# Performance work log

Hardware: AMD Instinct MI355X
Metric: run time of the kernel (lower is better)

## Reference

```python
import jax, jax.numpy as jnp
import numpy as np
from jax import lax

B, QL, VL, D, H, K = 8, 512, 2048, 1024, 8, 10
DH = D // H  # per-head dim = 128


def setup_inputs() -> dict:
    key = jax.random.key(0)
    ks = jax.random.split(key, 12)
    s = 0.02
    return {
        "Q": jax.random.normal(ks[0], (B, QL, D), jnp.float32),
        "V": jax.random.normal(ks[1], (B, VL, D), jnp.float32),
        "last_align": jax.random.uniform(ks[2], (B, QL), jnp.float32),
        "conv_w": jax.random.normal(ks[3], (K, 1, 3), jnp.float32) * s,
        "conv_b": jnp.zeros((K,), jnp.float32),
        "Wq": jax.random.normal(ks[4], (D, D), jnp.float32) * s,
        "bq": jnp.zeros((D,), jnp.float32),
        "Wv": jax.random.normal(ks[5], (D, D), jnp.float32) * s,
        "bv": jnp.zeros((D,), jnp.float32),
        "Wu": jax.random.normal(ks[6], (D, K), jnp.float32) * s,
        "bu": jnp.zeros((D,), jnp.float32),
        "bias": jax.random.uniform(ks[7], (D,), jnp.float32, -0.1, 0.1),
        "fc_w": jax.random.normal(ks[8], (D, 2 * D), jnp.float32) * s,
        "fc_b": jnp.zeros((D,), jnp.float32),
    }


def reference(Q, V, last_align, conv_w, conv_b, Wq, bq, Wv, bv, Wu, bu, bias, fc_w, fc_b):
    b, qlen, d_model = Q.shape
    vlen = V.shape[1]
    # location feature: conv1d over last_align -> (B, K, qlen) -> (B, qlen, K)
    u = lax.conv_general_dilated(last_align[:, None, :], conv_w, (1,), [(1, 1)],
                                 dimension_numbers=("NCH", "OIH", "NCH"))
    U = jnp.transpose(u + conv_b[None, :, None], (0, 2, 1))  # (B, qlen, K)
    # fused projections + bias adds
    q_s = Q @ Wq.T + bq + U @ Wu.T + bu + bias  # (B, qlen, D)
    v_s = V @ Wv.T + bv                          # (B, vlen, D)
    q_s = q_s.reshape(b, qlen, H, DH)
    v_s = v_s.reshape(b, vlen, H, DH)
    score = jnp.einsum("bqhd,bvhd->bhqv", q_s, v_s) / np.sqrt(DH).astype(jnp.float32)
    # sigmoid smoothing normalization (not softmax)
    score = jax.nn.sigmoid(score)
    align = score / jnp.sum(score, axis=-1, keepdims=True)  # (B, H, qlen, vlen)
    context = jnp.einsum("bhqv,bvhd->bqhd", align, v_s).reshape(b, qlen, d_model)
    combined = jnp.concatenate([context, Q], axis=-1)  # (B, qlen, 2D)
    output = jnp.tanh(combined @ fc_w.T + fc_b)        # (B, qlen, D)
    # torch returns align flattened head-major: (H*B, qlen, vlen)
    align_t = jnp.transpose(align, (1, 0, 2, 3)).reshape(H * b, qlen, vlen)
    return output, align_t
```

## Files before the change

kernel.cpp:

```cpp
#include <hip/hip_runtime.h>

typedef __attribute__((ext_vector_type(8))) short short8;
typedef __attribute__((ext_vector_type(4))) short short4v;
typedef __attribute__((ext_vector_type(4))) float f32x4;

static __device__ __forceinline__ short f2bf(float x) {
    unsigned u = __builtin_bit_cast(unsigned, x);
    unsigned r = (u + 0x7fffu + ((u >> 16) & 1u)) >> 16;
    return (short)r;
}

static __device__ __forceinline__ void gld16(const short* g, short* l) {
    __builtin_amdgcn_global_load_lds((const __attribute__((address_space(1))) void*)g,
                                     (__attribute__((address_space(3))) void*)l, 16, 0, 0);
}

#define QL 512
#define VL 2048
#define DM 1024
#define NH 8
#define DH 128
#define NB 8
#define KQ 1088

__global__ void cbias_k(const float* __restrict__ bq, const float* __restrict__ bu,
                        const float* __restrict__ bias, float* __restrict__ cbias) {
    int i = blockIdx.x * 256 + threadIdx.x;
    if (i < DM) cbias[i] = bq[i] + bu[i] + bias[i];
}

__global__ void conv_prep_k(const float* __restrict__ la, const float* __restrict__ cw,
                            const float* __restrict__ cb, short* __restrict__ Aq) {
    int m = blockIdx.x * 256 + threadIdx.x;
    if (m >= NB * QL) return;
    int b = m >> 9, t = m & 511;
    const float* l = la + b * QL;
    float lm = (t > 0)      ? l[t - 1] : 0.f;
    float l0 = l[t];
    float lp = (t < QL - 1) ? l[t + 1] : 0.f;
    short* row = Aq + (size_t)m * KQ + 1024;
#pragma unroll
    for (int k = 0; k < 10; ++k)
        row[k] = f2bf(cb[k] + lm * cw[k * 3 + 0] + l0 * cw[k * 3 + 1] + lp * cw[k * 3 + 2]);
    for (int k = 10; k < 64; ++k) row[k] = 0;
}

__global__ void castq_k(const float* __restrict__ Q, short* __restrict__ Aq,
                        short* __restrict__ comb) {
    int id = blockIdx.x * 256 + threadIdx.x;
    int m = id >> 7, kc = (id & 127) * 8;
    const float* p = Q + (size_t)m * DM + kc;
    float4 f0 = *(const float4*)p;
    float4 f1 = *(const float4*)(p + 4);
    short8 v;
    v[0]=f2bf(f0.x); v[1]=f2bf(f0.y); v[2]=f2bf(f0.z); v[3]=f2bf(f0.w);
    v[4]=f2bf(f1.x); v[5]=f2bf(f1.y); v[6]=f2bf(f1.z); v[7]=f2bf(f1.w);
    *(short8*)(Aq + (size_t)m * KQ + kc) = v;
    *(short8*)(comb + (size_t)m * (2 * DM) + DM + kc) = v;
}

__global__ void castv_k(const float* __restrict__ V, short* __restrict__ Vb) {
    int id = blockIdx.x * 256 + threadIdx.x;
    const float* p = V + (size_t)id * 8;
    float4 f0 = *(const float4*)p;
    float4 f1 = *(const float4*)(p + 4);
    short8 v;
    v[0]=f2bf(f0.x); v[1]=f2bf(f0.y); v[2]=f2bf(f0.z); v[3]=f2bf(f0.w);
    v[4]=f2bf(f1.x); v[5]=f2bf(f1.y); v[6]=f2bf(f1.z); v[7]=f2bf(f1.w);
    *(short8*)(Vb + (size_t)id * 8) = v;
}

__global__ void buildw_k(const float* __restrict__ Wq, const float* __restrict__ Wu,
                         const float* __restrict__ Wv, const float* __restrict__ fcw,
                         short* __restrict__ Bq, short* __restrict__ Bv, short* __restrict__ Bfc) {
    int id = blockIdx.x * 256 + threadIdx.x;
    const int nq = DM * KQ;
    const int nv = DM * DM;
    const int nf = DM * 2 * DM;
    if (id < nq) {
        int n = id / KQ, k = id % KQ;
        float v = (k < 1024) ? Wq[(size_t)n * 1024 + k]
                             : ((k < 1034) ? Wu[n * 10 + (k - 1024)] : 0.f);
        Bq[id] = f2bf(v);
    } else if (id < nq + nv) {
        int j = id - nq;
        Bv[j] = f2bf(Wv[j]);
    } else if (id < nq + nv + nf) {
        int j = id - nq - nv;
        Bfc[j] = f2bf(fcw[j]);
    }
}

template <int MODE>
__global__ __launch_bounds__(256) void gemm2_k(
    const short* __restrict__ A, const short* __restrict__ B,
    const float* __restrict__ bias, void* __restrict__ out0,
    short* __restrict__ outT, int M, int N, int K, int out_ld) {
    __shared__ short As[128 * 64];
    __shared__ short Bs[128 * 64];
    const int tid = threadIdx.x;
    const int lane = tid & 63, wave = tid >> 6;
    const int g = lane >> 4, c = lane & 15;
    const int nbm = M >> 7;
    const int x = blockIdx.x & 7, j = blockIdx.x >> 3;
    const int bm = x * (nbm >> 3) + (j >> 3);
    const int bn = j & 7;
    const int wr = wave >> 1, wc = wave & 1;

    const int srow = lane >> 3, scol = (lane & 7) * 8;
    const short* ag = A + (size_t)(bm * 128 + wave * 32 + srow) * K + scol;
    const short* bg = B + (size_t)(bn * 128 + wave * 32 + srow) * K + scol;

    f32x4 acc[4][4] = {};
    for (int k0 = 0; k0 < K; k0 += 64) {
#pragma unroll
        for (int ch = 0; ch < 4; ++ch) {
            gld16(ag + (size_t)(ch * 8) * K + k0, As + (wave * 32 + ch * 8) * 64);
            gld16(bg + (size_t)(ch * 8) * K + k0, Bs + (wave * 32 + ch * 8) * 64);
        }
        __syncthreads();
#pragma unroll
        for (int ks = 0; ks < 2; ++ks) {
            short8 af[4], bfr[4];
#pragma unroll
            for (int mi = 0; mi < 4; ++mi) af[mi] = *(const short8*)(As + (wr * 64 + mi * 16 + c) * 64 + ks * 32 + g * 8);
#pragma unroll
            for (int ni = 0; ni < 4; ++ni) bfr[ni] = *(const short8*)(Bs + (wc * 64 + ni * 16 + c) * 64 + ks * 32 + g * 8);
#pragma unroll
            for (int mi = 0; mi < 4; ++mi)
#pragma unroll
                for (int ni = 0; ni < 4; ++ni)
                    acc[mi][ni] = __builtin_amdgcn_mfma_f32_16x16x32_bf16(af[mi], bfr[ni], acc[mi][ni], 0, 0, 0);
        }
        __syncthreads();
    }

    const int m0 = bm * 128 + wr * 64, n0 = bn * 128 + wc * 64;
#pragma unroll
    for (int ni = 0; ni < 4; ++ni) {
        int n = n0 + ni * 16 + c;
        float bn_ = bias[n];
#pragma unroll
        for (int mi = 0; mi < 4; ++mi) {
            int mb = m0 + mi * 16 + 4 * g;
            f32x4 v = acc[mi][ni];
            if constexpr (MODE == 2) {
                float* o = (float*)out0;
#pragma unroll
                for (int r = 0; r < 4; ++r)
                    o[(size_t)(mb + r) * out_ld + n] = tanhf(v[r] + bn_);
            } else {
                short* o = (short*)out0;
                short4v pk;
#pragma unroll
                for (int r = 0; r < 4; ++r) {
                    pk[r] = f2bf(v[r] + bn_);
                    o[(size_t)(mb + r) * out_ld + n] = pk[r];
                }
                if constexpr (MODE == 0) {
                    int h = n >> 7, hd = n & 127;
                    int bb = mb >> 11, vv = mb & 2047;
                    *(short4v*)(outT + ((size_t)((bb * NH + h) * DH + hd)) * VL + vv) = pk;
                }
            }
        }
    }
}

__global__ __launch_bounds__(256) void rowsum_k(
    const short* __restrict__ qs, const short* __restrict__ vs,
    float* __restrict__ rsum_part) {
    __shared__ short As[128 * 64];
    __shared__ short Bs[128 * 64];
    const int blk = blockIdx.x;
    const int xr = blk & 7, t = blk >> 3;
    const int bn = t & 15;
    const int bm = (t >> 4) & 3;
    const int bh = ((t >> 6) << 3) | xr;
    const int h = bh & 7, b = bh >> 3;

    const int tid = threadIdx.x;
    const int lane = tid & 63, wave = tid >> 6;
    const int g = lane >> 4, c = lane & 15;
    const int wr = wave >> 1, wc = wave & 1;
    const float sc = 0.08838834764831845f;

    const int srow = lane >> 3, scol = (lane & 7) * 8;
    const short* ag = qs + (size_t)(b * QL + bm * 128 + wave * 32 + srow) * DM + h * DH + scol;
    const short* bg = vs + (size_t)(b * VL + bn * 128 + wave * 32 + srow) * DM + h * DH + scol;

    f32x4 acc[4][4] = {};
    for (int k0 = 0; k0 < DH; k0 += 64) {
#pragma unroll
        for (int ch = 0; ch < 4; ++ch) {
            gld16(ag + (size_t)(ch * 8) * DM + k0, As + (wave * 32 + ch * 8) * 64);
            gld16(bg + (size_t)(ch * 8) * DM + k0, Bs + (wave * 32 + ch * 8) * 64);
        }
        __syncthreads();
#pragma unroll
        for (int ks = 0; ks < 2; ++ks) {
            short8 af[4], bfr[4];
#pragma unroll
            for (int mi = 0; mi < 4; ++mi) af[mi] = *(const short8*)(As + (wr * 64 + mi * 16 + c) * 64 + ks * 32 + g * 8);
#pragma unroll
            for (int ni = 0; ni < 4; ++ni) bfr[ni] = *(const short8*)(Bs + (wc * 64 + ni * 16 + c) * 64 + ks * 32 + g * 8);
#pragma unroll
            for (int mi = 0; mi < 4; ++mi)
#pragma unroll
                for (int ni = 0; ni < 4; ++ni)
                    acc[mi][ni] = __builtin_amdgcn_mfma_f32_16x16x32_bf16(af[mi], bfr[ni], acc[mi][ni], 0, 0, 0);
        }
        __syncthreads();
    }

    float psum[4][4];
#pragma unroll
    for (int mi = 0; mi < 4; ++mi)
#pragma unroll
        for (int r = 0; r < 4; ++r) psum[mi][r] = 0.f;

    const int m0 = bm * 128 + wr * 64;
#pragma unroll
    for (int ni = 0; ni < 4; ++ni) {
#pragma unroll
        for (int mi = 0; mi < 4; ++mi) {
            f32x4 v = acc[mi][ni];
#pragma unroll
            for (int r = 0; r < 4; ++r)
                psum[mi][r] += __builtin_amdgcn_rcpf(1.f + __expf(-v[r] * sc));
        }
    }
#pragma unroll
    for (int off = 1; off < 16; off <<= 1)
#pragma unroll
        for (int mi = 0; mi < 4; ++mi)
#pragma unroll
            for (int r = 0; r < 4; ++r) psum[mi][r] += __shfl_xor(psum[mi][r], off);
    if (c == 0) {
#pragma unroll
        for (int mi = 0; mi < 4; ++mi)
#pragma unroll
            for (int r = 0; r < 4; ++r) {
                int q = m0 + mi * 16 + 4 * g + r;
                rsum_part[(size_t)(bh * QL + q) * 32 + bn * 2 + wc] = psum[mi][r];
            }
    }
}

__global__ __launch_bounds__(256) void fat_k(
    const short* __restrict__ qs, const short* __restrict__ vs,
    const short* __restrict__ vsT, const float* __restrict__ rsum_part,
    float* __restrict__ align_out, short* __restrict__ comb) {
    __shared__ short Vs[64][136];
    __shared__ short Vt[128][72];
    __shared__ short Pl[4][16][72];
    __shared__ float rsl[64];

    const int blk = blockIdx.x;
    const int xr = blk & 7, t = blk >> 3;
    const int qt = t & 7;
    const int bh = ((t >> 3) << 3) | xr;
    const int h = bh & 7, b = bh >> 3;
    const int q0 = qt * 64;

    const int tid = threadIdx.x, wave = tid >> 6, lane = tid & 63;
    const int g = lane >> 4, c = lane & 15;
    const float sc = 0.08838834764831845f;

    if (tid < 64) {
        const float* p = rsum_part + (size_t)(bh * QL + q0 + tid) * 32;
        float s = 0.f;
#pragma unroll
        for (int jj = 0; jj < 32; ++jj) s += p[jj];
        rsl[tid] = __builtin_amdgcn_rcpf(s);
    }
    __syncthreads();

    float invr[4];
#pragma unroll
    for (int r = 0; r < 4; ++r) invr[r] = rsl[wave * 16 + 4 * g + r];

    short8 qa[4];
    const short* qb = qs + ((size_t)(b * QL + q0 + wave * 16 + c)) * DM + h * DH + g * 8;
#pragma unroll
    for (int ks = 0; ks < 4; ++ks) qa[ks] = *(const short8*)(qb + ks * 32);

    const int vsrow = tid >> 2, vscq = (tid & 3) * 32;
    const short* vsg = vs + ((size_t)(b * VL + vsrow)) * DM + h * DH + vscq;
    const int vtrow = tid >> 1, vtcq = (tid & 1) * 32;
    const short* vtg = vsT + ((size_t)(bh * DH + vtrow)) * VL + vtcq;

    float* ao = align_out + ((size_t)((h * NB + b) * QL + q0 + wave * 16)) * VL;

    f32x4 ctx[8] = {};
    for (int v0 = 0; v0 < VL; v0 += 64) {
#pragma unroll
        for (int i = 0; i < 4; ++i)
            *(short8*)&Vs[vsrow][vscq + i * 8] = *(const short8*)(vsg + (size_t)v0 * DM + i * 8);
#pragma unroll
        for (int i = 0; i < 4; ++i)
            *(short8*)&Vt[vtrow][vtcq + i * 8] = *(const short8*)(vtg + v0 + i * 8);
        __syncthreads();

#pragma unroll
        for (int ni = 0; ni < 4; ++ni) {
            f32x4 s = {0.f, 0.f, 0.f, 0.f};
#pragma unroll
            for (int ks = 0; ks < 4; ++ks)
                s = __builtin_amdgcn_mfma_f32_16x16x32_bf16(qa[ks], *(const short8*)&Vs[ni * 16 + c][ks * 32 + g * 8], s, 0, 0, 0);
#pragma unroll
            for (int r = 0; r < 4; ++r) {
                float pn = __builtin_amdgcn_rcpf(1.f + __expf(-s[r] * sc)) * invr[r];
                __builtin_nontemporal_store(pn, &ao[(size_t)(4 * g + r) * VL + v0 + ni * 16 + c]);
                Pl[wave][4 * g + r][ni * 16 + c] = f2bf(pn);
            }
        }
        short8 pa0 = *(const short8*)&Pl[wave][c][g * 8];
        short8 pa1 = *(const short8*)&Pl[wave][c][32 + g * 8];
#pragma unroll
        for (int df = 0; df < 8; ++df) {
            ctx[df] = __builtin_amdgcn_mfma_f32_16x16x32_bf16(pa0, *(const short8*)&Vt[df * 16 + c][g * 8], ctx[df], 0, 0, 0);
            ctx[df] = __builtin_amdgcn_mfma_f32_16x16x32_bf16(pa1, *(const short8*)&Vt[df * 16 + c][32 + g * 8], ctx[df], 0, 0, 0);
        }
        __syncthreads();
    }

#pragma unroll
    for (int df = 0; df < 8; ++df)
#pragma unroll
        for (int r = 0; r < 4; ++r)
            comb[((size_t)(b * QL + q0 + wave * 16 + 4 * g + r)) * (2 * DM) + h * DH + df * 16 + c] = f2bf(ctx[df][r]);
}

extern "C" void kernel_launch(void* const* d_in, const int* in_sizes, int n_in,
                              void* d_out, int out_size, void* d_ws, size_t ws_size,
                              hipStream_t stream) {
    (void)in_sizes; (void)n_in; (void)out_size; (void)ws_size;
    const float* Q    = (const float*)d_in[0];
    const float* V    = (const float*)d_in[1];
    const float* la   = (const float*)d_in[2];
    const float* cw   = (const float*)d_in[3];
    const float* cb   = (const float*)d_in[4];
    const float* Wq   = (const float*)d_in[5];
    const float* bq   = (const float*)d_in[6];
    const float* Wv   = (const float*)d_in[7];
    const float* bv   = (const float*)d_in[8];
    const float* Wu   = (const float*)d_in[9];
    const float* bu   = (const float*)d_in[10];
    const float* bias = (const float*)d_in[11];
    const float* fcw  = (const float*)d_in[12];
    const float* fcb  = (const float*)d_in[13];

    float* out = (float*)d_out;
    float* align_out = out + (size_t)NB * QL * DM;

    char* w = (char*)d_ws;
    char* R0 = w;                        w += (size_t)33554432;
    short* Vb    = (short*)R0;
    short* Aq    = (short*)R0;
    short* comb  = (short*)(R0 + 8912896);
    float* cbias = (float*)(R0 + 8912896 + 16777216);
    short* Bq   = (short*)w; w += (size_t)1024 * KQ * 2;
    short* Bvw  = (short*)w; w += (size_t)1024 * 1024 * 2;
    short* Bfc  = (short*)w; w += (size_t)1024 * 2048 * 2;
    short* vsb  = (short*)w; w += (size_t)16384 * 1024 * 2;
    short* vsT  = (short*)w; w += (size_t)16384 * 1024 * 2;
    short* qsb  = (short*)w; w += (size_t)4096 * 1024 * 2;
    float* rsum_part = (float*)w; w += (size_t)32768 * 32 * 4;

    castv_k<<<8192, 256, 0, stream>>>(V, Vb);
    {
        int total = 1024 * KQ + 1024 * 1024 + 1024 * 2048;
        buildw_k<<<(total + 255) / 256, 256, 0, stream>>>(Wq, Wu, Wv, fcw, Bq, Bvw, Bfc);
    }
    gemm2_k<0><<<1024, 256, 0, stream>>>(Vb, Bvw, bv, vsb, vsT, 16384, 1024, 1024, 1024);
    cbias_k<<<4, 256, 0, stream>>>(bq, bu, bias, cbias);
    conv_prep_k<<<16, 256, 0, stream>>>(la, cw, cb, Aq);
    castq_k<<<2048, 256, 0, stream>>>(Q, Aq, comb);
    gemm2_k<1><<<256, 256, 0, stream>>>(Aq, Bq, cbias, qsb, nullptr, 4096, 1024, KQ, 1024);
    rowsum_k<<<4096, 256, 0, stream>>>(qsb, vsb, rsum_part);
    fat_k<<<512, 256, 0, stream>>>(qsb, vsb, vsT, rsum_part, align_out, comb);
    gemm2_k<2><<<256, 256, 0, stream>>>(comb, Bfc, fcb, out, nullptr, 4096, 1024, 2048, 1024);
}
```

Measured before the change: 355.7 us.

## Merge prep kernels, split fat kernel over V halves with register prefetch

The five small preparation kernels become one launch that dispatches on block index, cutting launch overhead and serialisation. The fused attention kernel now splits the value length into two halves, doubling the grid from 512 to 1024 blocks, and sets a launch bound of three blocks per CU. The next V tile is prefetched into registers while the current one is computed. Partial contexts are written as fp32 to a new workspace and summed by a new reduction kernel, which adds extra global traffic and one more launch.

Measured after the change: 311.4 us. -12.5%, faster.

```diff
diff --git a/kernel.cpp b/kernel.cpp
--- a/kernel.cpp
+++ b/kernel.cpp
@@ -23,71 +23,71 @@
 #define NB 8
 #define KQ 1088
 
-__global__ void cbias_k(const float* __restrict__ bq, const float* __restrict__ bu,
-                        const float* __restrict__ bias, float* __restrict__ cbias) {
-    int i = blockIdx.x * 256 + threadIdx.x;
-    if (i < DM) cbias[i] = bq[i] + bu[i] + bias[i];
-}
-
-__global__ void conv_prep_k(const float* __restrict__ la, const float* __restrict__ cw,
-                            const float* __restrict__ cb, short* __restrict__ Aq) {
-    int m = blockIdx.x * 256 + threadIdx.x;
-    if (m >= NB * QL) return;
-    int b = m >> 9, t = m & 511;
-    const float* l = la + b * QL;
-    float lm = (t > 0)      ? l[t - 1] : 0.f;
-    float l0 = l[t];
-    float lp = (t < QL - 1) ? l[t + 1] : 0.f;
-    short* row = Aq + (size_t)m * KQ + 1024;
-#pragma unroll
-    for (int k = 0; k < 10; ++k)
-        row[k] = f2bf(cb[k] + lm * cw[k * 3 + 0] + l0 * cw[k * 3 + 1] + lp * cw[k * 3 + 2]);
-    for (int k = 10; k < 64; ++k) row[k] = 0;
-}
-
-__global__ void castq_k(const float* __restrict__ Q, short* __restrict__ Aq,
-                        short* __restrict__ comb) {
-    int id = blockIdx.x * 256 + threadIdx.x;
-    int m = id >> 7, kc = (id & 127) * 8;
-    const float* p = Q + (size_t)m * DM + kc;
-    float4 f0 = *(const float4*)p;
-    float4 f1 = *(const float4*)(p + 4);
-    short8 v;
-    v[0]=f2bf(f0.x); v[1]=f2bf(f0.y); v[2]=f2bf(f0.z); v[3]=f2bf(f0.w);
-    v[4]=f2bf(f1.x); v[5]=f2bf(f1.y); v[6]=f2bf(f1.z); v[7]=f2bf(f1.w);
-    *(short8*)(Aq + (size_t)m * KQ + kc) = v;
-    *(short8*)(comb + (size_t)m * (2 * DM) + DM + kc) = v;
-}
-
-__global__ void castv_k(const float* __restrict__ V, short* __restrict__ Vb) {
-    int id = blockIdx.x * 256 + threadIdx.x;
-    const float* p = V + (size_t)id * 8;
-    float4 f0 = *(const float4*)p;
-    float4 f1 = *(const float4*)(p + 4);
-    short8 v;
-    v[0]=f2bf(f0.x); v[1]=f2bf(f0.y); v[2]=f2bf(f0.z); v[3]=f2bf(f0.w);
-    v[4]=f2bf(f1.x); v[5]=f2bf(f1.y); v[6]=f2bf(f1.z); v[7]=f2bf(f1.w);
-    *(short8*)(Vb + (size_t)id * 8) = v;
-}
-
-__global__ void buildw_k(const float* __restrict__ Wq, const float* __restrict__ Wu,
-                         const float* __restrict__ Wv, const float* __restrict__ fcw,
-                         short* __restrict__ Bq, short* __restrict__ Bv, short* __restrict__ Bfc) {
-    int id = blockIdx.x * 256 + threadIdx.x;
-    const int nq = DM * KQ;
-    const int nv = DM * DM;
-    const int nf = DM * 2 * DM;
-    if (id < nq) {
-        int n = id / KQ, k = id % KQ;
-        float v = (k < 1024) ? Wq[(size_t)n * 1024 + k]
-                             : ((k < 1034) ? Wu[n * 10 + (k - 1024)] : 0.f);
-        Bq[id] = f2bf(v);
-    } else if (id < nq + nv) {
-        int j = id - nq;
-        Bv[j] = f2bf(Wv[j]);
-    } else if (id < nq + nv + nf) {
-        int j = id - nq - nv;
-        Bfc[j] = f2bf(fcw[j]);
+__global__ void prep_k(const float* __restrict__ Q, const float* __restrict__ V,
+                       const float* __restrict__ la, const float* __restrict__ cw,
+                       const float* __restrict__ cb,
+                       const float* __restrict__ Wq, const float* __restrict__ bq,
+                       const float* __restrict__ Wv, const float* __restrict__ Wu,
+                       const float* __restrict__ bu, const float* __restrict__ bias,
+                       const float* __restrict__ fcw,
+                       float* __restrict__ cbias, short* __restrict__ Aq,
+                       short* __restrict__ comb, short* __restrict__ Vb,
+                       short* __restrict__ Bq, short* __restrict__ Bv,
+                       short* __restrict__ Bfc) {
+    const int blk = blockIdx.x, tid = threadIdx.x;
+    if (blk < 4) {
+        int i = blk * 256 + tid;
+        if (i < DM) cbias[i] = bq[i] + bu[i] + bias[i];
+    } else if (blk < 20) {
+        int m = (blk - 4) * 256 + tid;
+        if (m >= NB * QL) return;
+        int b = m >> 9, t = m & 511;
+        const float* l = la + b * QL;
+        float lm = (t > 0)      ? l[t - 1] : 0.f;
+        float l0 = l[t];
+        float lp = (t < QL - 1) ? l[t + 1] : 0.f;
+        short* row = Aq + (size_t)m * KQ + 1024;
+#pragma unroll
+        for (int k = 0; k < 10; ++k)
+            row[k] = f2bf(cb[k] + lm * cw[k * 3 + 0] + l0 * cw[k * 3 + 1] + lp * cw[k * 3 + 2]);
+        for (int k = 10; k < 64; ++k) row[k] = 0;
+    } else if (blk < 2068) {
+        int id = (blk - 20) * 256 + tid;
+        int m = id >> 7, kc = (id & 127) * 8;
+        const float* p = Q + (size_t)m * DM + kc;
+        float4 f0 = *(const float4*)p;
+        float4 f1 = *(const float4*)(p + 4);
+        short8 v;
+        v[0]=f2bf(f0.x); v[1]=f2bf(f0.y); v[2]=f2bf(f0.z); v[3]=f2bf(f0.w);
+        v[4]=f2bf(f1.x); v[5]=f2bf(f1.y); v[6]=f2bf(f1.z); v[7]=f2bf(f1.w);
+        *(short8*)(Aq + (size_t)m * KQ + kc) = v;
+        *(short8*)(comb + (size_t)m * (2 * DM) + DM + kc) = v;
+    } else if (blk < 10260) {
+        int id = (blk - 2068) * 256 + tid;
+        const float* p = V + (size_t)id * 8;
+        float4 f0 = *(const float4*)p;
+        float4 f1 = *(const float4*)(p + 4);
+        short8 v;
+        v[0]=f2bf(f0.x); v[1]=f2bf(f0.y); v[2]=f2bf(f0.z); v[3]=f2bf(f0.w);
+        v[4]=f2bf(f1.x); v[5]=f2bf(f1.y); v[6]=f2bf(f1.z); v[7]=f2bf(f1.w);
+        *(short8*)(Vb + (size_t)id * 8) = v;
+    } else {
+        int id = (blk - 10260) * 256 + tid;
+        const int nq = DM * KQ;
+        const int nv = DM * DM;
+        const int nf = DM * 2 * DM;
+        if (id < nq) {
+            int n = id / KQ, k = id % KQ;
+            float v = (k < 1024) ? Wq[(size_t)n * 1024 + k]
+                                 : ((k < 1034) ? Wu[n * 10 + (k - 1024)] : 0.f);
+            Bq[id] = f2bf(v);
+        } else if (id < nq + nv) {
+            int j = id - nq;
+            Bv[j] = f2bf(Wv[j]);
+        } else if (id < nq + nv + nf) {
+            int j = id - nq - nv;
+            Bfc[j] = f2bf(fcw[j]);
+        }
     }
 }
 
@@ -247,10 +247,10 @@
     }
 }
 
-__global__ __launch_bounds__(256) void fat_k(
+__global__ __launch_bounds__(256, 3) void fat2_k(
     const short* __restrict__ qs, const short* __restrict__ vs,
     const short* __restrict__ vsT, const float* __restrict__ rsum_part,
-    float* __restrict__ align_out, short* __restrict__ comb) {
+    float* __restrict__ align_out, float* __restrict__ ctxp) {
     __shared__ short Vs[64][136];
     __shared__ short Vt[128][72];
     __shared__ short Pl[4][16][72];
@@ -258,10 +258,12 @@
 
     const int blk = blockIdx.x;
     const int xr = blk & 7, t = blk >> 3;
-    const int qt = t & 7;
-    const int bh = ((t >> 3) << 3) | xr;
+    const int vh = t & 1;
+    const int qt = (t >> 1) & 7;
+    const int bh = ((t >> 4) << 3) | xr;
     const int h = bh & 7, b = bh >> 3;
     const int q0 = qt * 64;
+    const int vbeg = vh * 1024;
 
     const int tid = threadIdx.x, wave = tid >> 6, lane = tid & 63;
     const int g = lane >> 4, c = lane & 15;
@@ -292,15 +294,27 @@
 
     float* ao = align_out + ((size_t)((h * NB + b) * QL + q0 + wave * 16)) * VL;
 
+    short8 pv_s[4], pv_t[4];
+#pragma unroll
+    for (int i = 0; i < 4; ++i) pv_s[i] = *(const short8*)(vsg + (size_t)vbeg * DM + i * 8);
+#pragma unroll
+    for (int i = 0; i < 4; ++i) pv_t[i] = *(const short8*)(vtg + vbeg + i * 8);
+
     f32x4 ctx[8] = {};
-    for (int v0 = 0; v0 < VL; v0 += 64) {
-#pragma unroll
-        for (int i = 0; i < 4; ++i)
-            *(short8*)&Vs[vsrow][vscq + i * 8] = *(const short8*)(vsg + (size_t)v0 * DM + i * 8);
-#pragma unroll
-        for (int i = 0; i < 4; ++i)
-            *(short8*)&Vt[vtrow][vtcq + i * 8] = *(const short8*)(vtg + v0 + i * 8);
-        __syncthreads();
+    for (int tc = 0; tc < 16; ++tc) {
+        const int v0 = vbeg + tc * 64;
+#pragma unroll
+        for (int i = 0; i < 4; ++i) *(short8*)&Vs[vsrow][vscq + i * 8] = pv_s[i];
+#pragma unroll
+        for (int i = 0; i < 4; ++i) *(short8*)&Vt[vtrow][vtcq + i * 8] = pv_t[i];
+        __syncthreads();
+        if (tc + 1 < 16) {
+            const int v1 = v0 + 64;
+#pragma unroll
+            for (int i = 0; i < 4; ++i) pv_s[i] = *(const short8*)(vsg + (size_t)v1 * DM + i * 8);
+#pragma unroll
+            for (int i = 0; i < 4; ++i) pv_t[i] = *(const short8*)(vtg + v1 + i * 8);
+        }
 
 #pragma unroll
         for (int ni = 0; ni < 4; ++ni) {
@@ -325,11 +339,27 @@
         __syncthreads();
     }
 
+    float* cp = ctxp + ((size_t)((bh * 8 + qt) * 2 + vh)) * (64 * 128);
 #pragma unroll
     for (int df = 0; df < 8; ++df)
 #pragma unroll
         for (int r = 0; r < 4; ++r)
-            comb[((size_t)(b * QL + q0 + wave * 16 + 4 * g + r)) * (2 * DM) + h * DH + df * 16 + c] = f2bf(ctx[df][r]);
+            cp[(size_t)(wave * 16 + 4 * g + r) * 128 + df * 16 + c] = ctx[df][r];
+}
+
+__global__ void ctxred_k(const float* __restrict__ ctxp, short* __restrict__ comb) {
+    int id = blockIdx.x * 256 + threadIdx.x;
+    int d0 = (id & 15) * 8;
+    int r  = (id >> 4) & 63;
+    int qt = (id >> 10) & 7;
+    int bh = id >> 13;
+    int h = bh & 7, b = bh >> 3;
+    const float* p0 = ctxp + ((size_t)((bh * 8 + qt) * 2)) * 8192 + r * 128 + d0;
+    const float* p1 = p0 + 8192;
+    short8 o;
+#pragma unroll
+    for (int jj = 0; jj < 8; ++jj) o[jj] = f2bf(p0[jj] + p1[jj]);
+    *(short8*)(comb + ((size_t)(b * QL + qt * 64 + r)) * (2 * DM) + h * DH + d0) = o;
 }
 
 extern "C" void kernel_launch(void* const* d_in, const int* in_sizes, int n_in,
@@ -355,11 +385,9 @@
     float* align_out = out + (size_t)NB * QL * DM;
 
     char* w = (char*)d_ws;
-    char* R0 = w;                        w += (size_t)33554432;
-    short* Vb    = (short*)R0;
-    short* Aq    = (short*)R0;
-    short* comb  = (short*)(R0 + 8912896);
-    float* cbias = (float*)(R0 + 8912896 + 16777216);
+    short* Vb   = (short*)w; w += (size_t)16384 * 1024 * 2;
+    short* Aq   = (short*)w; w += (size_t)4096 * KQ * 2;
+    short* comb = (short*)w; w += (size_t)4096 * 2048 * 2;
     short* Bq   = (short*)w; w += (size_t)1024 * KQ * 2;
     short* Bvw  = (short*)w; w += (size_t)1024 * 1024 * 2;
     short* Bfc  = (short*)w; w += (size_t)1024 * 2048 * 2;
@@ -367,18 +395,15 @@
     short* vsT  = (short*)w; w += (size_t)16384 * 1024 * 2;
     short* qsb  = (short*)w; w += (size_t)4096 * 1024 * 2;
     float* rsum_part = (float*)w; w += (size_t)32768 * 32 * 4;
-
-    castv_k<<<8192, 256, 0, stream>>>(V, Vb);
-    {
-        int total = 1024 * KQ + 1024 * 1024 + 1024 * 2048;
-        buildw_k<<<(total + 255) / 256, 256, 0, stream>>>(Wq, Wu, Wv, fcw, Bq, Bvw, Bfc);
-    }
+    float* ctxp = (float*)w; w += (size_t)1024 * 64 * 128 * 4;
+    float* cbias = (float*)w; w += 1024 * 4;
+
+    prep_k<<<26900, 256, 0, stream>>>(Q, V, la, cw, cb, Wq, bq, Wv, Wu, bu, bias, fcw,
+                                      cbias, Aq, comb, Vb, Bq, Bvw, Bfc);
     gemm2_k<0><<<1024, 256, 0, stream>>>(Vb, Bvw, bv, vsb, vsT, 16384, 1024, 1024, 1024);
-    cbias_k<<<4, 256, 0, stream>>>(bq, bu, bias, cbias);
-    conv_prep_k<<<16, 256, 0, stream>>>(la, cw, cb, Aq);
-    castq_k<<<2048, 256, 0, stream>>>(Q, Aq, comb);
     gemm2_k<1><<<256, 256, 0, stream>>>(Aq, Bq, cbias, qsb, nullptr, 4096, 1024, KQ, 1024);
     rowsum_k<<<4096, 256, 0, stream>>>(qsb, vsb, rsum_part);
-    fat_k<<<512, 256, 0, stream>>>(qsb, vsb, vsT, rsum_part, align_out, comb);
+    fat2_k<<<1024, 256, 0, stream>>>(qsb, vsb, vsT, rsum_part, align_out, ctxp);
+    ctxred_k<<<2048, 256, 0, stream>>>(ctxp, comb);
     gemm2_k<2><<<256, 256, 0, stream>>>(comb, Bfc, fcb, out, nullptr, 4096, 1024, 2048, 1024);
 }
```
